# Optimization experiments

Hardware: AMD Instinct MI355X
Metric: run time of the kernel (lower is better)

The kernel has to match this reference:

```python
import jax, jax.numpy as jnp
import numpy as np

N_NODES = 100000
N_EDGES = 1600000
NEG_SLOPE = 0.2
EPS = 1e-16


def gat_conv(x, edge_index, W, att_src, att_dst, bias, heads, out_ch, concat):
    # x: [N, F_in]; edge_index: [2, E] with edge (src j -> dst i)
    N = x.shape[0]
    src, dst = edge_index[0], edge_index[1]
    h = (x @ W).reshape(N, heads, out_ch)              # [N, H, C]
    a_src = (h * att_src[None]).sum(-1)                # [N, H]
    a_dst = (h * att_dst[None]).sum(-1)                # [N, H]
    e = a_src[src] + a_dst[dst]                        # [E, H]
    e = jnp.where(e > 0, e, NEG_SLOPE * e)             # LeakyReLU(0.2)
    # segment softmax over destination node
    m = jax.ops.segment_max(e, dst, num_segments=N)    # [N, H]
    m = jnp.where(jnp.isfinite(m), m, 0.0)
    ex = jnp.exp(e - m[dst])                           # [E, H]
    s = jax.ops.segment_sum(ex, dst, num_segments=N)   # [N, H]
    alpha = ex / (s[dst] + EPS)                        # [E, H]
    msg = h[src] * alpha[..., None]                    # [E, H, C]
    out = jax.ops.segment_sum(msg, dst, num_segments=N)  # [N, H, C]
    if concat:
        out = out.reshape(N, heads * out_ch)
    else:
        out = out.mean(axis=1)
    return out + bias


def setup_inputs() -> dict:
    key = jax.random.key(0)
    ks = jax.random.split(key, 8)
    x = jax.random.normal(ks[0], (N_NODES, 2), dtype=jnp.float32)
    edge_index = jax.random.randint(ks[1], (2, N_EDGES), 0, N_NODES, dtype=jnp.int64)
    glorot = lambda k, shape, fan: jax.random.normal(k, shape, jnp.float32) * (1.0 / np.sqrt(fan))
    W1 = glorot(ks[2], (2, 128), 2)
    att_src1 = glorot(ks[3], (8, 16), 16)
    att_dst1 = glorot(ks[4], (8, 16), 16)
    b1 = jnp.zeros((128,), jnp.float32)
    W2 = glorot(ks[5], (128, 4), 128)
    att_src2 = glorot(ks[6], (1, 4), 4)
    att_dst2 = glorot(ks[7], (1, 4), 4)
    b2 = jnp.zeros((4,), jnp.float32)
    return {"x": x, "edge_index": edge_index, "W1": W1, "att_src1": att_src1,
            "att_dst1": att_dst1, "b1": b1, "W2": W2, "att_src2": att_src2,
            "att_dst2": att_dst2, "b2": b2}


def reference(x, edge_index, W1, att_src1, att_dst1, b1, W2, att_src2, att_dst2, b2):
    h = gat_conv(x, edge_index, W1, att_src1, att_dst1, b1, heads=8, out_ch=16, concat=True)
    h = jax.nn.relu(h)
    # dropout p=0.6 is identity in eval mode
    h = gat_conv(h, edge_index, W2, att_src2, att_dst2, b2, heads=1, out_ch=4, concat=True)
    return jax.nn.log_softmax(h, axis=1)
```

## Files before the change

kernel.cpp:

```cpp
#include <hip/hip_runtime.h>
#include <math.h>

static constexpr float kNegSlope = 0.2f;
static constexpr float kEps = 1e-16f;
static constexpr int SLICES = 256;
static constexpr int BSHIFT = 7;
static constexpr int BMASK = 127;
static constexpr unsigned SRCMASK = 0x1FFFFu;
static constexpr int CAP = 2816;

__device__ __forceinline__ float leaky(float v) {
    return v > 0.0f ? v : kNegSlope * v;
}


__global__ __launch_bounds__(512) void k_hist1(const int* __restrict__ ei,
                                               int* __restrict__ table,
                                               int* __restrict__ rowptr,
                                               int E, int N, int NBUCK) {
    __shared__ int hist[832];
    int b = blockIdx.x, t = threadIdx.x;
    if (b == 0 && t == 0) rowptr[N] = E;
    for (int i = t; i < NBUCK; i += 512) hist[i] = 0;
    __syncthreads();
    int S = (((E + SLICES - 1) / SLICES) + 3) & ~3;
    int lo = b * S, hi = min(lo + S, E);
    for (int i = lo + t * 4; i < hi; i += 512 * 4) {
        int4 dv = *(const int4*)(ei + E + i);
        atomicAdd(&hist[dv.x >> BSHIFT], 1);
        atomicAdd(&hist[dv.y >> BSHIFT], 1);
        atomicAdd(&hist[dv.z >> BSHIFT], 1);
        atomicAdd(&hist[dv.w >> BSHIFT], 1);
    }
    __syncthreads();
    for (int i = t; i < NBUCK; i += 512) table[i * SLICES + b] = hist[i];
}

__global__ __launch_bounds__(256) void k_scan_reduce(const int* __restrict__ src,
                                                     int* __restrict__ partial, int n) {
    __shared__ int wsum[4];
    int b = blockIdx.x, t = threadIdx.x;
    int base = b * 1024 + t * 4;
    int s = 0;
#pragma unroll
    for (int k = 0; k < 4; ++k) {
        int idx = base + k;
        s += (idx < n) ? src[idx] : 0;
    }
#pragma unroll
    for (int off = 1; off < 64; off <<= 1) s += __shfl_xor(s, off);
    if ((t & 63) == 0) wsum[t >> 6] = s;
    __syncthreads();
    if (t == 0) partial[b] = wsum[0] + wsum[1] + wsum[2] + wsum[3];
}

__global__ __launch_bounds__(256) void k_scan_apply(int* __restrict__ data,
                                                    const int* __restrict__ partial,
                                                    int n, int nsb) {
    __shared__ int sm[8];
    __shared__ int baseSh;
    int b = blockIdx.x, t = threadIdx.x;
    int acc = 0;
    for (int i = t; i < b; i += 256) acc += partial[i];
#pragma unroll
    for (int off = 1; off < 64; off <<= 1) acc += __shfl_xor(acc, off);
    if ((t & 63) == 0) sm[t >> 6] = acc;
    __syncthreads();
    if (t == 0) baseSh = sm[0] + sm[1] + sm[2] + sm[3];
    __syncthreads();
    int chunkBase = baseSh;
    __syncthreads();
    int base = b * 1024 + t * 4;
    int v[4];
#pragma unroll
    for (int k = 0; k < 4; ++k) {
        int idx = base + k;
        v[k] = (idx < n) ? data[idx] : 0;
    }
    int sum4 = v[0] + v[1] + v[2] + v[3];
    int s = sum4;
#pragma unroll
    for (int off = 1; off < 64; off <<= 1) {
        int u = __shfl_up(s, off);
        if ((t & 63) >= off) s += u;
    }
    if ((t & 63) == 63) sm[t >> 6] = s;
    __syncthreads();
    int woff = 0;
    int w = t >> 6;
    for (int ww = 0; ww < w; ++ww) woff += sm[ww];
    int ex = chunkBase + woff + (s - sum4);
#pragma unroll
    for (int k = 0; k < 4; ++k) {
        int idx = base + k;
        if (idx < n) data[idx] = ex;
        ex += v[k];
    }
}

__global__ __launch_bounds__(512) void k_bin2(const int* __restrict__ ei,
                                              const int* __restrict__ table,
                                              unsigned* __restrict__ sbuf, int E, int NBUCK) {
    __shared__ int cur[832];
    int b = blockIdx.x, t = threadIdx.x;
    for (int i = t; i < NBUCK; i += 512) cur[i] = table[i * SLICES + b];
    __syncthreads();
    int S = (((E + SLICES - 1) / SLICES) + 3) & ~3;
    int lo = b * S, hi = min(lo + S, E);
    for (int i = lo + t * 4; i < hi; i += 512 * 4) {
        int4 sv = *(const int4*)(ei + i);
        int4 dv = *(const int4*)(ei + E + i);
        int pos;
        pos = atomicAdd(&cur[dv.x >> BSHIFT], 1);
        sbuf[pos] = (unsigned)sv.x | ((unsigned)(dv.x & BMASK) << 17);
        pos = atomicAdd(&cur[dv.y >> BSHIFT], 1);
        sbuf[pos] = (unsigned)sv.y | ((unsigned)(dv.y & BMASK) << 17);
        pos = atomicAdd(&cur[dv.z >> BSHIFT], 1);
        sbuf[pos] = (unsigned)sv.z | ((unsigned)(dv.z & BMASK) << 17);
        pos = atomicAdd(&cur[dv.w >> BSHIFT], 1);
        sbuf[pos] = (unsigned)sv.w | ((unsigned)(dv.w & BMASK) << 17);
    }
}

__global__ __launch_bounds__(512) void k_sort(
        const unsigned* __restrict__ sbuf, const int* __restrict__ table,
        int* __restrict__ rowptr, int* __restrict__ ssrc,
        int N, int E, int NBUCK) {
    __shared__ int hist[128];
    __shared__ int sc[128];
    __shared__ int cur[128];
    __shared__ unsigned raws[CAP];
    __shared__ int sls[CAP];
    int b = blockIdx.x;
    int t = threadIdx.x;
    int lo = table[b * SLICES];
    int hi = (b + 1 < NBUCK) ? table[(b + 1) * SLICES] : E;
    int cnt = hi - lo;
    bool inLds = (cnt <= CAP);

    if (t < 128) hist[t] = 0;
    __syncthreads();

    if (inLds) {
        for (int i = t; i < cnt; i += 512) {
            unsigned v = sbuf[lo + i];
            raws[i] = v;
            atomicAdd(&hist[v >> 17], 1);
        }
    } else {
        for (int i = lo + t; i < hi; i += 512) atomicAdd(&hist[sbuf[i] >> 17], 1);
    }
    __syncthreads();

    if (t < 128) {
        int lane = t & 63;
        int own = hist[t];
        int v = own;
#pragma unroll
        for (int off = 1; off < 64; off <<= 1) {
            int u = __shfl_up(v, off);
            if (lane >= off) v += u;
        }
        sc[t] = v;
    }
    __syncthreads();
    if (t < 128) {
        int ex = sc[t] - hist[t] + (t >= 64 ? sc[63] : 0);
        cur[t] = ex;
        int node = (b << BSHIFT) + t;
        if (node < N) rowptr[node] = lo + ex;
    }
    __syncthreads();

    if (inLds) {
        for (int i = t; i < cnt; i += 512) {
            unsigned v = raws[i];
            int pos = atomicAdd(&cur[v >> 17], 1);
            sls[pos] = (int)(v & SRCMASK);
        }
        __syncthreads();
        for (int i = t; i < cnt; i += 512) ssrc[lo + i] = sls[i];
    } else {
        for (int i = lo + t; i < hi; i += 512) {
            unsigned v = sbuf[i];
            int pos = atomicAdd(&cur[v >> 17], 1);
            ssrc[lo + pos] = (int)(v & SRCMASK);
        }
    }
}

__global__ __launch_bounds__(256) void k_gather1(
        const int* __restrict__ rowptr, const int* __restrict__ ssrc,
        const float* __restrict__ x,
        const float* __restrict__ W1, const float* __restrict__ att_src1,
        const float* __restrict__ att_dst1, const float* __restrict__ b1,
        const float* __restrict__ W2, float* __restrict__ h2, int N) {
    __shared__ float pbuf[32];
    int t = threadIdx.x;
    if (t < 32) {
        int which = t >> 4;
        int hd = t & 15;
        int h = hd >> 1, d = hd & 1;
        const float* att = which ? att_dst1 : att_src1;
        float s = 0.0f;
#pragma unroll
        for (int c = 0; c < 16; ++c) s += W1[d * 128 + h * 16 + c] * att[h * 16 + c];
        pbuf[which * 16 + d * 8 + h] = s;
    }
    __syncthreads();

    int idx = blockIdx.x * blockDim.x + t;
    int n = idx >> 3, q = idx & 7;
    if (n >= N) return;
    const float2* x2 = (const float2*)x;
    int start = rowptr[n], end = rowptr[n + 1];
    float2 xn = x2[n];
    float Ps0[8], Ps1[8], adv[8], l[8], s0[8], s1[8];
#pragma unroll
    for (int h = 0; h < 8; ++h) {
        Ps0[h] = pbuf[h];
        Ps1[h] = pbuf[8 + h];
        adv[h] = xn.x * pbuf[16 + h] + xn.y * pbuf[24 + h];
        l[h] = 0.f; s0[h] = 0.f; s1[h] = 0.f;
    }
    for (int j = start + q; j < end; j += 8) {
        int src = ssrc[j];
        float2 xs = x2[src];
#pragma unroll
        for (int h = 0; h < 8; ++h) {
            float p = __expf(leaky(xs.x * Ps0[h] + xs.y * Ps1[h] + adv[h]));
            l[h] += p; s0[h] += p * xs.x; s1[h] += p * xs.y;
        }
    }
#pragma unroll
    for (int off = 1; off < 8; off <<= 1) {
#pragma unroll
        for (int h = 0; h < 8; ++h) {
            l[h] += __shfl_xor(l[h], off);
            s0[h] += __shfl_xor(s0[h], off);
            s1[h] += __shfl_xor(s1[h], off);
        }
    }
    float h0 = 0.f, h1v = 0.f, h2v = 0.f, h3 = 0.f;
    {
        float inv = 1.0f / (l[q] + kEps);
        float sX0 = s0[q] * inv, sX1 = s1[q] * inv;
#pragma unroll
        for (int c = 0; c < 16; ++c) {
            int col = q * 16 + c;
            float o = fmaxf(W1[col] * sX0 + W1[128 + col] * sX1 + b1[col], 0.0f);
            h0 += o * W2[col * 4 + 0];
            h1v += o * W2[col * 4 + 1];
            h2v += o * W2[col * 4 + 2];
            h3 += o * W2[col * 4 + 3];
        }
    }
#pragma unroll
    for (int off = 1; off < 8; off <<= 1) {
        h0 += __shfl_xor(h0, off);
        h1v += __shfl_xor(h1v, off);
        h2v += __shfl_xor(h2v, off);
        h3 += __shfl_xor(h3, off);
    }
    if (q == 0) {
        ((float4*)h2)[n] = make_float4(h0, h1v, h2v, h3);
    }
}

__global__ __launch_bounds__(256) void k_gather2_out(
        const int* __restrict__ rowptr, const int* __restrict__ ssrc,
        const float* __restrict__ h2, const float* __restrict__ att_src2,
        const float* __restrict__ att_dst2, const float* __restrict__ b2,
        float* __restrict__ out, int N) {
    int idx = blockIdx.x * blockDim.x + threadIdx.x;
    int n = idx >> 3, q = idx & 7;
    if (n >= N) return;
    int start = rowptr[n], end = rowptr[n + 1];
    float4 as2 = *(const float4*)att_src2;
    float4 ad2v = *(const float4*)att_dst2;
    float4 hn = ((const float4*)h2)[n];
    float ad = hn.x * ad2v.x + hn.y * ad2v.y + hn.z * ad2v.z + hn.w * ad2v.w;
    float l = 0.0f;
    float4 acc = make_float4(0.f, 0.f, 0.f, 0.f);
    for (int j = start + q; j < end; j += 8) {
        int src = ssrc[j];
        float4 hv = ((const float4*)h2)[src];
        float e = hv.x * as2.x + hv.y * as2.y + hv.z * as2.z + hv.w * as2.w + ad;
        float p = __expf(leaky(e));
        l += p;
        acc.x += p * hv.x; acc.y += p * hv.y; acc.z += p * hv.z; acc.w += p * hv.w;
    }
#pragma unroll
    for (int off = 1; off < 8; off <<= 1) {
        l += __shfl_xor(l, off);
        acc.x += __shfl_xor(acc.x, off);
        acc.y += __shfl_xor(acc.y, off);
        acc.z += __shfl_xor(acc.z, off);
        acc.w += __shfl_xor(acc.w, off);
    }
    if (q == 0) {
        float inv = 1.0f / (l + kEps);
        float4 v = make_float4(acc.x * inv + b2[0], acc.y * inv + b2[1],
                               acc.z * inv + b2[2], acc.w * inv + b2[3]);
        float mx = fmaxf(fmaxf(v.x, v.y), fmaxf(v.z, v.w));
        float sum = __expf(v.x - mx) + __expf(v.y - mx) + __expf(v.z - mx) + __expf(v.w - mx);
        float lse = mx + logf(sum);
        ((float4*)out)[n] = make_float4(v.x - lse, v.y - lse, v.z - lse, v.w - lse);
    }
}

extern "C" void kernel_launch(void* const* d_in, const int* in_sizes, int n_in,
                              void* d_out, int out_size, void* d_ws, size_t ws_size,
                              hipStream_t stream) {
    const float* x        = (const float*)d_in[0];
    const int*   ei       = (const int*)d_in[1];
    const float* W1       = (const float*)d_in[2];
    const float* att_src1 = (const float*)d_in[3];
    const float* att_dst1 = (const float*)d_in[4];
    const float* b1       = (const float*)d_in[5];
    const float* W2       = (const float*)d_in[6];
    const float* att_src2 = (const float*)d_in[7];
    const float* att_dst2 = (const float*)d_in[8];
    const float* b2       = (const float*)d_in[9];

    const int N = in_sizes[0] / 2;
    const int E = in_sizes[1] / 2;
    const int NBUCK = (N + BMASK) >> BSHIFT;
    const int ntable = NBUCK * SLICES;
    const int nsb = (ntable + 1023) / 1024;

    int* table     = (int*)d_ws;
    int* partial   = table + ntable + 64;
    int* rowptr    = partial + 1024;
    int* ssrc      = rowptr + ((N + 4) & ~3);
    unsigned* sbuf = (unsigned*)(ssrc + E);
    float* h2      = (float*)(sbuf + E);

    k_hist1<<<SLICES, 512, 0, stream>>>(ei, table, rowptr, E, N, NBUCK);
    k_scan_reduce<<<nsb, 256, 0, stream>>>(table, partial, ntable);
    k_scan_apply<<<nsb, 256, 0, stream>>>(table, partial, ntable, nsb);
    k_bin2<<<SLICES, 512, 0, stream>>>(ei, table, sbuf, E, NBUCK);

    k_sort<<<NBUCK, 512, 0, stream>>>(sbuf, table, rowptr, ssrc, N, E, NBUCK);

    k_gather1<<<(N * 8 + 255) / 256, 256, 0, stream>>>(rowptr, ssrc, x,
                                                       W1, att_src1, att_dst1, b1,
                                                       W2, h2, N);

    k_gather2_out<<<(N * 8 + 255) / 256, 256, 0, stream>>>(rowptr, ssrc, h2,
                                                           att_src2, att_dst2, b2,
                                                           (float*)d_out, N);
}
```

Baseline: 164.4 us.

## Pre-gather source features into edge-ordered buffer and unroll layer-2 gather loop

Adds a kernel that materializes x[src] for every sorted edge into a contiguous float2 array, reusing the sort scratch buffer. The layer-1 gather then reads it sequentially instead of doing an index load followed by a random load. The layer-2 gather loop is unrolled by two to keep more independent loads in flight. The cost is an extra kernel launch and an extra pass over E edges with its own random reads and writes, and the workspace layout now pads E.

```diff
diff --git a/kernel.cpp b/kernel.cpp
--- a/kernel.cpp
+++ b/kernel.cpp
@@ -189,8 +189,30 @@
     }
 }
 
+__global__ __launch_bounds__(256) void k_fill(const int* __restrict__ ssrc,
+                                              const float* __restrict__ x,
+                                              float* __restrict__ sxy, int E) {
+    int i4 = (blockIdx.x * 256 + threadIdx.x) * 4;
+    const float2* x2 = (const float2*)x;
+    if (i4 + 3 < E) {
+        int4 s = *(const int4*)(ssrc + i4);
+        float2 a = x2[s.x];
+        float2 b = x2[s.y];
+        float2 c = x2[s.z];
+        float2 d = x2[s.w];
+        *(float4*)(sxy + 2 * i4)     = make_float4(a.x, a.y, b.x, b.y);
+        *(float4*)(sxy + 2 * i4 + 4) = make_float4(c.x, c.y, d.x, d.y);
+    } else {
+        for (int i = i4; i < E; ++i) {
+            float2 a = x2[ssrc[i]];
+            sxy[2 * i] = a.x;
+            sxy[2 * i + 1] = a.y;
+        }
+    }
+}
+
 __global__ __launch_bounds__(256) void k_gather1(
-        const int* __restrict__ rowptr, const int* __restrict__ ssrc,
+        const int* __restrict__ rowptr, const float* __restrict__ sxy,
         const float* __restrict__ x,
         const float* __restrict__ W1, const float* __restrict__ att_src1,
         const float* __restrict__ att_dst1, const float* __restrict__ b1,
@@ -213,6 +235,7 @@
     int n = idx >> 3, q = idx & 7;
     if (n >= N) return;
     const float2* x2 = (const float2*)x;
+    const float2* sx2 = (const float2*)sxy;
     int start = rowptr[n], end = rowptr[n + 1];
     float2 xn = x2[n];
     float Ps0[8], Ps1[8], adv[8], l[8], s0[8], s1[8];
@@ -224,8 +247,7 @@
         l[h] = 0.f; s0[h] = 0.f; s1[h] = 0.f;
     }
     for (int j = start + q; j < end; j += 8) {
-        int src = ssrc[j];
-        float2 xs = x2[src];
+        float2 xs = sx2[j];
 #pragma unroll
         for (int h = 0; h < 8; ++h) {
             float p = __expf(leaky(xs.x * Ps0[h] + xs.y * Ps1[h] + adv[h]));
@@ -278,17 +300,37 @@
     int start = rowptr[n], end = rowptr[n + 1];
     float4 as2 = *(const float4*)att_src2;
     float4 ad2v = *(const float4*)att_dst2;
-    float4 hn = ((const float4*)h2)[n];
+    const float4* h4 = (const float4*)h2;
+    float4 hn = h4[n];
     float ad = hn.x * ad2v.x + hn.y * ad2v.y + hn.z * ad2v.z + hn.w * ad2v.w;
     float l = 0.0f;
     float4 acc = make_float4(0.f, 0.f, 0.f, 0.f);
-    for (int j = start + q; j < end; j += 8) {
-        int src = ssrc[j];
-        float4 hv = ((const float4*)h2)[src];
-        float e = hv.x * as2.x + hv.y * as2.y + hv.z * as2.z + hv.w * as2.w + ad;
-        float p = __expf(leaky(e));
-        l += p;
-        acc.x += p * hv.x; acc.y += p * hv.y; acc.z += p * hv.z; acc.w += p * hv.w;
+    int j = start + q;
+    for (; j + 8 < end; j += 16) {
+        int s0 = ssrc[j];
+        int s1 = ssrc[j + 8];
+        float4 ha = h4[s0];
+        float4 hb = h4[s1];
+        float e0 = ha.x * as2.x + ha.y * as2.y + ha.z * as2.z + ha.w * as2.w + ad;
+        float e1 = hb.x * as2.x + hb.y * as2.y + hb.z * as2.z + hb.w * as2.w + ad;
+        float p0 = __expf(leaky(e0));
+        float p1 = __expf(leaky(e1));
+        l += p0 + p1;
+        acc.x += p0 * ha.x + p1 * hb.x;
+        acc.y += p0 * ha.y + p1 * hb.y;
+        acc.z += p0 * ha.z + p1 * hb.z;
+        acc.w += p0 * ha.w + p1 * hb.w;
+    }
+    if (j < end) {
+        int s0 = ssrc[j];
+        float4 ha = h4[s0];
+        float e0 = ha.x * as2.x + ha.y * as2.y + ha.z * as2.z + ha.w * as2.w + ad;
+        float p0 = __expf(leaky(e0));
+        l += p0;
+        acc.x += p0 * ha.x;
+        acc.y += p0 * ha.y;
+        acc.z += p0 * ha.z;
+        acc.w += p0 * ha.w;
     }
 #pragma unroll
     for (int off = 1; off < 8; off <<= 1) {
@@ -328,13 +370,15 @@
     const int NBUCK = (N + BMASK) >> BSHIFT;
     const int ntable = NBUCK * SLICES;
     const int nsb = (ntable + 1023) / 1024;
+    const int Epad = (E + 3) & ~3;
 
     int* table     = (int*)d_ws;
     int* partial   = table + ntable + 64;
     int* rowptr    = partial + 1024;
     int* ssrc      = rowptr + ((N + 4) & ~3);
-    unsigned* sbuf = (unsigned*)(ssrc + E);
-    float* h2      = (float*)(sbuf + E);
+    unsigned* sbuf = (unsigned*)(ssrc + Epad);
+    float* sxy     = (float*)sbuf;
+    float* h2      = (float*)((int*)sbuf + 2 * (size_t)Epad);
 
     k_hist1<<<SLICES, 512, 0, stream>>>(ei, table, rowptr, E, N, NBUCK);
     k_scan_reduce<<<nsb, 256, 0, stream>>>(table, partial, ntable);
@@ -343,7 +387,9 @@
 
     k_sort<<<NBUCK, 512, 0, stream>>>(sbuf, table, rowptr, ssrc, N, E, NBUCK);
 
-    k_gather1<<<(N * 8 + 255) / 256, 256, 0, stream>>>(rowptr, ssrc, x,
+    k_fill<<<((E + 3) / 4 + 255) / 256, 256, 0, stream>>>(ssrc, x, sxy, E);
+
+    k_gather1<<<(N * 8 + 255) / 256, 256, 0, stream>>>(rowptr, sxy, x,
                                                        W1, att_src1, att_dst1, b1,
                                                        W2, h2, N);
 
```

New measurement: 172.7 us. 5.0% more time.
